# Kernel optimization log

Hardware: AMD Instinct MI355X
Metric: run time of the kernel (lower is better)

## Reference

```python
import jax, jax.numpy as jnp
import numpy as np
import math

B, S, D = 1, 2048, 2048
H, HD, KV = 16, 128, 1
E, F, TOPK = 8, 4096, 2
EPS = 1e-5


def setup_inputs() -> dict:
    key = jax.random.key(0)
    ks = jax.random.split(key, 14)
    sc = 0.02
    inp = {
        "x": jax.random.normal(ks[0], (B, S, D), dtype=jnp.float32),
        "wq": jax.random.normal(ks[1], (D, H * HD), dtype=jnp.float32) * sc,
        "wk": jax.random.normal(ks[2], (D, KV * HD), dtype=jnp.float32) * sc,
        "wv": jax.random.normal(ks[3], (D, KV * HD), dtype=jnp.float32) * sc,
        "wo": jax.random.normal(ks[4], (H * HD, D), dtype=jnp.float32) * sc,
        "w_router": jax.random.normal(ks[5], (D, E), dtype=jnp.float32) * sc,
        "w1": jax.random.normal(ks[6], (E, D, F), dtype=jnp.float32) * sc,
        "w3": jax.random.normal(ks[7], (E, D, F), dtype=jnp.float32) * sc,
        "w2": jax.random.normal(ks[8], (E, F, D), dtype=jnp.float32) * sc,
        "s_pre_mqa": jnp.ones((D,), dtype=jnp.float32),
        "s_post_mqa": jnp.ones((D,), dtype=jnp.float32),
        "s_pre_moe": jnp.ones((D,), dtype=jnp.float32),
        "s_post_moe": jnp.ones((D,), dtype=jnp.float32),
    }
    return inp


def _rmsnorm(x, scale):
    ms = jnp.mean(x * x, axis=-1, keepdims=True)
    return x * jax.lax.rsqrt(ms + EPS) * scale


def _mqa(h, wq, wk, wv, wo):
    b, s, _ = h.shape
    q = (h @ wq).reshape(b, s, H, HD)
    k = (h @ wk).reshape(b, s, KV, HD)
    v = (h @ wv).reshape(b, s, KV, HD)
    # repeat_interleave kv heads up to H (MQA)
    k = jnp.repeat(k, H // KV, axis=2)
    v = jnp.repeat(v, H // KV, axis=2)
    scale = 1.0 / math.sqrt(HD)
    scores = jnp.einsum("bqhd,bkhd->bhqk", q, k) * scale  # [B,H,S,S]
    causal = jnp.tril(jnp.ones((s, s), dtype=bool))
    scores = jnp.where(causal, scores, jnp.float32(-jnp.inf))
    attn = jax.nn.softmax(scores, axis=-1)
    out = jnp.einsum("bhqk,bkhd->bqhd", attn, v).reshape(b, s, H * HD)
    return out @ wo


def _moe(h, w_router, w1, w2, w3):
    logits = h @ w_router                        # [B,S,E]
    probs = jax.nn.softmax(logits, axis=-1)
    topv, topi = jax.lax.top_k(probs, TOPK)      # [B,S,K]
    topv = topv / jnp.sum(topv, axis=-1, keepdims=True)
    # combine weights per expert: [B,S,E]
    combine = jnp.sum(jax.nn.one_hot(topi, E, dtype=h.dtype) * topv[..., None], axis=-2)
    out = jnp.zeros_like(h)
    for e in range(E):  # fixed small expert count
        ye = (jax.nn.silu(h @ w1[e]) * (h @ w3[e])) @ w2[e]
        out = out + combine[..., e:e + 1] * ye
    return out, combine


def reference(x, wq, wk, wv, wo, w_router, w1, w2, w3,
              s_pre_mqa, s_post_mqa, s_pre_moe, s_post_moe):
    mqa_out = _mqa(_rmsnorm(x, s_pre_mqa), wq, wk, wv, wo)
    x = x + _rmsnorm(mqa_out, s_post_mqa)  # dropout p=0 (eval)
    moe_out, router_mask = _moe(_rmsnorm(x, s_pre_moe), w_router, w1, w2, w3)
    x = x + _rmsnorm(moe_out, s_post_moe)
    return x, router_mask
```

## Files before the change

kernel.cpp:

```cpp
#include <hip/hip_runtime.h>

#define S_LEN 2048
#define DM 2048
#define NHEAD 16
#define HDIM 128
#define NEXP 8
#define FF 4096
#define EPSV 1e-5f

typedef unsigned short u16;
typedef short bf16x8 __attribute__((ext_vector_type(8)));
typedef float f32x4 __attribute__((ext_vector_type(4)));

__device__ __forceinline__ f32x4 mfma16(bf16x8 a, bf16x8 b, f32x4 c) {
  return __builtin_amdgcn_mfma_f32_16x16x32_bf16(a, b, c, 0, 0, 0);
}

__device__ __forceinline__ float bf2f(u16 u) {
  union { unsigned int i; float f; } v; v.i = ((unsigned int)u) << 16; return v.f;
}
__device__ __forceinline__ u16 f2bf(float f) {
  union { float f; unsigned int i; } v; v.f = f;
  unsigned int u = v.i;
  return (u16)((u + 0x7fffu + ((u >> 16) & 1u)) >> 16);
}

__device__ __forceinline__ void gload_lds16(const u16* g, u16* l) {
  __builtin_amdgcn_global_load_lds(
      (const __attribute__((address_space(1))) unsigned int*)(unsigned long long)g,
      (__attribute__((address_space(3))) unsigned int*)(unsigned long long)l, 16, 0, 0);
}

__device__ __forceinline__ float blocksum(float v, float* sh) {
#pragma unroll
  for (int off = 32; off; off >>= 1) v += __shfl_xor(v, off, 64);
  const int w = threadIdx.x >> 6;
  if ((threadIdx.x & 63) == 0) sh[w] = v;
  __syncthreads();
  v = sh[0] + sh[1] + sh[2] + sh[3];
  __syncthreads();
  return v;
}

__device__ __forceinline__ void convsplit_body(char* lds, const float* __restrict__ src,
                                               int ld, u16* __restrict__ dhi,
                                               u16* __restrict__ dlo, int nblk, int kblk) {
  float(*tile)[65] = reinterpret_cast<float(*)[65]>(lds);
  const int n0 = nblk * 64, k0 = kblk * 64;
  const int t = threadIdx.x;
  {
    int r = t >> 4, c4 = (t & 15) * 4;
#pragma unroll
    for (int i = 0; i < 4; ++i) {
      float4 v = *reinterpret_cast<const float4*>(src + (size_t)(k0 + r + i * 16) * ld + n0 + c4);
      tile[r + i * 16][c4 + 0] = v.x;
      tile[r + i * 16][c4 + 1] = v.y;
      tile[r + i * 16][c4 + 2] = v.z;
      tile[r + i * 16][c4 + 3] = v.w;
    }
  }
  __syncthreads();
#pragma unroll
  for (int i = 0; i < 2; ++i) {
    int idx = i * 256 + t;
    int n = idx >> 3, kc = (idx & 7) * 8;
    bf16x8 hi, lo;
#pragma unroll
    for (int j = 0; j < 8; ++j) {
      float f = tile[kc + j][n];
      u16 hv = f2bf(f);
      hi[j] = (short)hv;
      lo[j] = (short)f2bf(f - bf2f(hv));
    }
    size_t o = (size_t)(n0 + n) * 2048 + k0 + kc;
    *reinterpret_cast<bf16x8*>(dhi + o) = hi;
    *reinterpret_cast<bf16x8*>(dlo + o) = lo;
  }
}

__device__ __forceinline__ void convT_body(char* lds, const float* __restrict__ src,
                                           int R, int C, u16* __restrict__ dst,
                                           int nblk, int rblk, int e) {
  float(*tile)[65] = reinterpret_cast<float(*)[65]>(lds);
  const int n0 = nblk * 64, r0 = rblk * 64;
  const size_t bofs = (size_t)e * R * C;
  const int t = threadIdx.x;
  {
    int r = t >> 4, c4 = (t & 15) * 4;
#pragma unroll
    for (int i = 0; i < 4; ++i) {
      float4 v = *reinterpret_cast<const float4*>(src + bofs + (size_t)(r0 + r + i * 16) * C + n0 + c4);
      tile[r + i * 16][c4 + 0] = v.x;
      tile[r + i * 16][c4 + 1] = v.y;
      tile[r + i * 16][c4 + 2] = v.z;
      tile[r + i * 16][c4 + 3] = v.w;
    }
  }
  __syncthreads();
#pragma unroll
  for (int i = 0; i < 2; ++i) {
    int idx = i * 256 + t;
    int n = idx >> 3, kc = (idx & 7) * 8;
    bf16x8 pk;
#pragma unroll
    for (int j = 0; j < 8; ++j) pk[j] = (short)f2bf(tile[kc + j][n]);
    *reinterpret_cast<bf16x8*>(dst + bofs + (size_t)(n0 + n) * R + r0 + kc) = pk;
  }
}

__device__ __forceinline__ void convT_body512(char* lds, const float* __restrict__ src,
                                              int R, int C, u16* __restrict__ dst,
                                              int nblk, int rblk, int e) {
  float(*tile)[65] = reinterpret_cast<float(*)[65]>(lds);
  const int n0 = nblk * 64, r0 = rblk * 64;
  const size_t bofs = (size_t)e * R * C;
  const int t = threadIdx.x;
#pragma unroll
  for (int i = 0; i < 2; ++i) {
    int p = i * 512 + t;
    int r = p >> 4, c4 = (p & 15) * 4;
    float4 v = *reinterpret_cast<const float4*>(src + bofs + (size_t)(r0 + r) * C + n0 + c4);
    tile[r][c4 + 0] = v.x;
    tile[r][c4 + 1] = v.y;
    tile[r][c4 + 2] = v.z;
    tile[r][c4 + 3] = v.w;
  }
  __syncthreads();
  {
    int n = t >> 3, kc = (t & 7) * 8;
    bf16x8 pk;
#pragma unroll
    for (int j = 0; j < 8; ++j) pk[j] = (short)f2bf(tile[kc + j][n]);
    *reinterpret_cast<bf16x8*>(dst + bofs + (size_t)(n0 + n) * R + r0 + kc) = pk;
  }
}

__device__ __forceinline__ void rms_pre_body(char* lds, const float* __restrict__ x,
                                             const float* __restrict__ s,
                                             u16* __restrict__ h1, int row) {
  float* sh = (float*)lds;
  const int t = threadIdx.x;
  const float* xr = x + (size_t)row * DM + t * 8;
  float4 a = *reinterpret_cast<const float4*>(xr);
  float4 b = *reinterpret_cast<const float4*>(xr + 4);
  float v[8] = {a.x, a.y, a.z, a.w, b.x, b.y, b.z, b.w};
  float ss = 0.f;
#pragma unroll
  for (int j = 0; j < 8; ++j) ss += v[j] * v[j];
  float inv = rsqrtf(blocksum(ss, sh) * (1.f / DM) + EPSV);
  const float* sp = s + t * 8;
  bf16x8 hi, lo;
#pragma unroll
  for (int j = 0; j < 8; ++j) {
    float val = v[j] * inv * sp[j];
    u16 hv = f2bf(val);
    hi[j] = (short)hv;
    lo[j] = (short)f2bf(val - bf2f(hv));
  }
  *reinterpret_cast<bf16x8*>(h1 + (size_t)row * 4096 + t * 8) = hi;
  *reinterpret_cast<bf16x8*>(h1 + (size_t)row * 4096 + 2048 + t * 8) = lo;
}

__global__ __launch_bounds__(256) void fat_pre(
    const float* __restrict__ x, const float* __restrict__ spre, u16* __restrict__ h1,
    const float* __restrict__ wq, const float* __restrict__ wk, const float* __restrict__ wv,
    u16* __restrict__ BtqHi, u16* __restrict__ BtqLo) {
  __shared__ alignas(16) char lds[16640];
  int bid = blockIdx.x;
  if (bid < 2048) {
    rms_pre_body(lds, x, spre, h1, bid);
  } else if (bid < 3072) {
    int c = bid - 2048;
    convsplit_body(lds, wq, 2048, BtqHi, BtqLo, c & 31, c >> 5);
  } else if (bid < 3136) {
    int c = bid - 3072;
    convsplit_body(lds, wk, 128, BtqHi + (size_t)2048 * 2048, BtqLo + (size_t)2048 * 2048,
                   c & 1, c >> 1);
  } else {
    int c = bid - 3136;
    convsplit_body(lds, wv, 128, BtqHi + (size_t)2176 * 2048, BtqLo + (size_t)2176 * 2048,
                   c & 1, c >> 1);
  }
}

__device__ __forceinline__ void gemm3_body(
    char* lds, const u16* __restrict__ A, const u16* __restrict__ Bthi,
    const u16* __restrict__ Btlo, void* __restrict__ out,
    int mblk, int nblk, int mode, int ldc, int lo_off) {
  const int m0 = mblk * 128, n0 = nblk * 64;
  const int t = threadIdx.x, lane = t & 63, w = t >> 6;
  const int wm = (w >> 1) * 64, wn = (w & 1) * 32;
  const int l15 = lane & 15, lg = lane >> 4;
  const int wbase = t & ~63;

  u16* Ah = (u16*)lds;
  u16* Al = (u16*)(lds + 16384);
  u16* Bh = (u16*)(lds + 32768);
  u16* Bl = (u16*)(lds + 40960);

  const u16* Abh = A + (size_t)m0 * 4096;
  const u16* Abl = Abh + 2048;
  const u16* Bbh = Bthi + (size_t)n0 * 2048;
  const u16* Bbl = Btlo + (size_t)n0 * 2048;

  f32x4 acc[4][2];
#pragma unroll
  for (int m = 0; m < 4; ++m)
#pragma unroll
    for (int n = 0; n < 2; ++n) acc[m][n] = (f32x4){0.f, 0.f, 0.f, 0.f};

  for (int k0 = 0; k0 < 2048; k0 += 64) {
    __syncthreads();
#pragma unroll
    for (int i = 0; i < 4; ++i) {
      int p = i * 256 + t;
      int row = p >> 3;
      int csrc = (p & 7) ^ (row & 7);
      gload_lds16(Abh + (size_t)row * 4096 + k0 + csrc * 8, Ah + (i * 256 + wbase) * 8);
      gload_lds16(Abl + (size_t)row * 4096 + k0 + csrc * 8, Al + (i * 256 + wbase) * 8);
    }
#pragma unroll
    for (int i = 0; i < 2; ++i) {
      int p = i * 256 + t;
      int row = p >> 3;
      int csrc = (p & 7) ^ (row & 7);
      gload_lds16(Bbh + (size_t)row * 2048 + k0 + csrc * 8, Bh + (i * 256 + wbase) * 8);
      gload_lds16(Bbl + (size_t)row * 2048 + k0 + csrc * 8, Bl + (i * 256 + wbase) * 8);
    }
    __syncthreads();
#pragma unroll
    for (int kk = 0; kk < 2; ++kk) {
      bf16x8 ah[4], al[4], bh[2], bl[2];
#pragma unroll
      for (int m = 0; m < 4; ++m) {
        int row = wm + m * 16 + l15;
        int byte = row * 128 + (((kk * 4 + lg) * 16) ^ ((row & 7) << 4));
        ah[m] = *reinterpret_cast<const bf16x8*>((const char*)Ah + byte);
        al[m] = *reinterpret_cast<const bf16x8*>((const char*)Al + byte);
      }
#pragma unroll
      for (int n = 0; n < 2; ++n) {
        int row = wn + n * 16 + l15;
        int byte = row * 128 + (((kk * 4 + lg) * 16) ^ ((row & 7) << 4));
        bh[n] = *reinterpret_cast<const bf16x8*>((const char*)Bh + byte);
        bl[n] = *reinterpret_cast<const bf16x8*>((const char*)Bl + byte);
      }
#pragma unroll
      for (int m = 0; m < 4; ++m)
#pragma unroll
        for (int n = 0; n < 2; ++n) {
          acc[m][n] = mfma16(ah[m], bh[n], acc[m][n]);
          acc[m][n] = mfma16(al[m], bh[n], acc[m][n]);
          acc[m][n] = mfma16(ah[m], bl[n], acc[m][n]);
        }
    }
  }
#pragma unroll
  for (int m = 0; m < 4; ++m)
#pragma unroll
    for (int n = 0; n < 2; ++n)
#pragma unroll
      for (int r = 0; r < 4; ++r) {
        int row = m0 + wm + m * 16 + lg * 4 + r;
        int col = n0 + wn + n * 16 + l15;
        float v = acc[m][n][r];
        if (mode == 1) {
          u16* C = (u16*)out;
          u16 hv = f2bf(v);
          C[(size_t)row * ldc + col] = hv;
          C[(size_t)row * ldc + lo_off + col] = f2bf(v - bf2f(hv));
        } else {
          ((float*)out)[(size_t)row * ldc + col] = v;
        }
      }
}

__global__ __launch_bounds__(256) void fat_qkv_conv(
    const u16* __restrict__ A, const u16* __restrict__ Bthi, const u16* __restrict__ Btlo,
    u16* __restrict__ QKV, const float* __restrict__ w1, u16* __restrict__ w1t,
    const float* __restrict__ wo, u16* __restrict__ BtoHi, u16* __restrict__ BtoLo) {
  __shared__ alignas(16) char lds[49152];
  int bid = blockIdx.x;
  if (bid < 576) {
    gemm3_body(lds, A, Bthi, Btlo, QKV, bid % 16, bid / 16, 1, 4608, 2304);
  } else {
    int cid = bid - 576;
    if (cid < 16384)
      convT_body(lds, w1, 2048, 4096, w1t, cid % 64, (cid / 64) % 32, cid / 2048);
    else {
      cid -= 16384;
      convsplit_body(lds, wo, 2048, BtoHi, BtoLo, cid & 31, cid >> 5);
    }
  }
}

__global__ __launch_bounds__(256) void vtrans_kernel(const u16* __restrict__ QKV,
                                                     u16* __restrict__ vt) {
  __shared__ u16 tile[64][65];
  const int s0 = blockIdx.x * 64, c0 = blockIdx.y * 64;
  const int t = threadIdx.x;
#pragma unroll
  for (int i = 0; i < 16; ++i) {
    int idx = i * 256 + t;
    int r = idx >> 6, c = idx & 63;
    int col = c0 + c;
    int src = (col < 128) ? (2176 + col) : (4480 + col - 128);
    tile[r][c] = QKV[(size_t)(s0 + r) * 4608 + src];
  }
  __syncthreads();
#pragma unroll
  for (int i = 0; i < 16; ++i) {
    int idx = i * 256 + t;
    int cc = idx >> 6, ss = idx & 63;
    vt[(size_t)(c0 + cc) * S_LEN + s0 + ss] = tile[ss][cc];
  }
}

__device__ __forceinline__ void attn_body(char* lds, const u16* __restrict__ QKV,
                                          const u16* __restrict__ vt, u16* __restrict__ Os,
                                          int bx, int h) {
  const int qb = 31 - bx;
  const int t = threadIdx.x, w = t >> 6, lane = t & 63;
  const int l15 = lane & 15, lg = lane >> 4;
  const int qr0 = qb * 64 + w * 16;
  const int qrow = qr0 + l15;

  u16* Ks = (u16*)lds;
  u16* Vs = (u16*)(lds + 17408);
  u16* myP = (u16*)(lds + 37888) + w * (16 * 72);

  bf16x8 qf[2][4];
#pragma unroll
  for (int p = 0; p < 2; ++p)
#pragma unroll
    for (int c = 0; c < 4; ++c)
      qf[p][c] = *reinterpret_cast<const bf16x8*>(QKV + (size_t)qrow * 4608 + p * 2304 +
                                                  h * 128 + c * 32 + lg * 8);

  f32x4 o[8];
#pragma unroll
  for (int n = 0; n < 8; ++n) o[n] = (f32x4){0.f, 0.f, 0.f, 0.f};
  f32x4 lracc = (f32x4){0.f, 0.f, 0.f, 0.f};
  bf16x8 onesf;
#pragma unroll
  for (int j = 0; j < 8; ++j) onesf[j] = (short)0x3F80;

  const float scale = 0.08838834764831845f;
  const int kend = qb * 64 + 64;

  for (int j0 = 0; j0 < kend; j0 += 32) {
    __syncthreads();
#pragma unroll
    for (int i = 0; i < 4; ++i) {
      int idx = i * 256 + t;
      int row = idx >> 5, seg = idx & 31;
      int srccol = (seg < 16) ? (2048 + seg * 8) : (4352 + (seg - 16) * 8);
      bf16x8 v = *reinterpret_cast<const bf16x8*>(QKV + (size_t)(j0 + row) * 4608 + srccol);
      *reinterpret_cast<bf16x8*>(&Ks[row * 272 + seg * 8]) = v;
    }
#pragma unroll
    for (int i = 0; i < 4; ++i) {
      int idx = i * 256 + t;
      int row = idx >> 2, seg = idx & 3;
      bf16x8 v = *reinterpret_cast<const bf16x8*>(vt + (size_t)row * S_LEN + j0 + seg * 8);
      *reinterpret_cast<bf16x8*>(&Vs[row * 40 + seg * 8]) = v;
    }
    __syncthreads();

    if (j0 > qr0 + 15) continue;
    f32x4 sc[2];
#pragma unroll
    for (int half = 0; half < 2; ++half) {
      const int kb = (half * 16 + l15) * 272;
      f32x4 a0 = (f32x4){0.f, 0.f, 0.f, 0.f};
      f32x4 a1 = (f32x4){0.f, 0.f, 0.f, 0.f};
      f32x4 a2 = (f32x4){0.f, 0.f, 0.f, 0.f};
#pragma unroll
      for (int cc = 0; cc < 4; ++cc) {
        bf16x8 kh = *reinterpret_cast<const bf16x8*>(&Ks[kb + cc * 32 + lg * 8]);
        a0 = mfma16(qf[0][cc], kh, a0);
        a1 = mfma16(qf[1][cc], kh, a1);
      }
#pragma unroll
      for (int cc = 0; cc < 4; ++cc) {
        bf16x8 kl = *reinterpret_cast<const bf16x8*>(&Ks[kb + 128 + cc * 32 + lg * 8]);
        a2 = mfma16(qf[0][cc], kl, a2);
      }
      f32x4 a = (a0 + a1) + a2;
#pragma unroll
      for (int r = 0; r < 4; ++r) {
        int rowg = qr0 + lg * 4 + r;
        int colg = j0 + half * 16 + l15;
        sc[half][r] = (colg <= rowg) ? a[r] * scale : -1e30f;
      }
    }
#pragma unroll
    for (int r = 0; r < 4; ++r) {
      float p0 = __expf(sc[0][r]);
      float p1 = __expf(sc[1][r]);
      int lrow = lg * 4 + r;
      u16 h0 = f2bf(p0), h1v = f2bf(p1);
      myP[lrow * 72 + l15] = h0;
      myP[lrow * 72 + 16 + l15] = h1v;
      myP[lrow * 72 + 32 + l15] = f2bf(p0 - bf2f(h0));
      myP[lrow * 72 + 48 + l15] = f2bf(p1 - bf2f(h1v));
    }
    bf16x8 pfh = *reinterpret_cast<const bf16x8*>(myP + l15 * 72 + lg * 8);
    bf16x8 pfl = *reinterpret_cast<const bf16x8*>(myP + l15 * 72 + 32 + lg * 8);

    lracc = mfma16(pfh, onesf, lracc);
    lracc = mfma16(pfl, onesf, lracc);

#pragma unroll
    for (int n = 0; n < 8; ++n) {
      bf16x8 vh = *reinterpret_cast<const bf16x8*>(&Vs[(n * 16 + l15) * 40 + lg * 8]);
      bf16x8 vl = *reinterpret_cast<const bf16x8*>(&Vs[(n * 16 + l15 + 128) * 40 + lg * 8]);
      o[n] = mfma16(pfh, vh, o[n]);
      o[n] = mfma16(pfl, vh, o[n]);
      o[n] = mfma16(pfh, vl, o[n]);
    }
  }
#pragma unroll
  for (int n = 0; n < 8; ++n)
#pragma unroll
    for (int r = 0; r < 4; ++r) {
      int rowg = qr0 + lg * 4 + r;
      float v = o[n][r] / lracc[r];
      u16 hv = f2bf(v);
      Os[(size_t)rowg * 4096 + h * 128 + n * 16 + l15] = hv;
      Os[(size_t)rowg * 4096 + 2048 + h * 128 + n * 16 + l15] = f2bf(v - bf2f(hv));
    }
}

__global__ __launch_bounds__(256) void fat_attn_conv(
    const u16* __restrict__ QKV, const u16* __restrict__ vt, u16* __restrict__ Os,
    const float* __restrict__ w3, u16* __restrict__ w3t) {
  __shared__ alignas(16) char lds[47104];
  int bid = blockIdx.x;
  if (bid < 512) {
    attn_body(lds, QKV, vt, Os, bid & 31, bid >> 5);
  } else {
    int cid = bid - 512;
    convT_body(lds, w3, 2048, 4096, w3t, cid % 64, (cid / 64) % 32, cid / 2048);
  }
}

__global__ __launch_bounds__(256) void fat_wo_conv(
    const u16* __restrict__ A, const u16* __restrict__ Bthi, const u16* __restrict__ Btlo,
    float* __restrict__ out, const float* __restrict__ w2, u16* __restrict__ w2t) {
  __shared__ alignas(16) char lds[49152];
  int bid = blockIdx.x;
  if (bid < 512) {
    gemm3_body(lds, A, Bthi, Btlo, out, bid & 15, bid >> 4, 2, 2048, 0);
  } else {
    int cid = bid - 512;
    convT_body(lds, w2, 4096, 2048, w2t, cid % 32, (cid / 32) % 64, cid / 2048);
  }
}

__global__ __launch_bounds__(256) void rms_mid_router(
    const float* __restrict__ x, const float* __restrict__ mqa,
    const float* __restrict__ spost, const float* __restrict__ spre,
    const float* __restrict__ wr, float* __restrict__ x1, u16* __restrict__ h2b,
    float* __restrict__ comb, int* __restrict__ topi, float* __restrict__ topw,
    int* __restrict__ cnt) {
  __shared__ float sh1[4];
  __shared__ float sh2[4];
  __shared__ float red[4][8];
  __shared__ float lgits[8];
  const int row = blockIdx.x, t = threadIdx.x;
  const size_t base = (size_t)row * DM + t * 8;
  float mv[8];
  {
    float4 a0 = *reinterpret_cast<const float4*>(mqa + base);
    float4 b0 = *reinterpret_cast<const float4*>(mqa + base + 4);
    mv[0] = a0.x; mv[1] = a0.y; mv[2] = a0.z; mv[3] = a0.w;
    mv[4] = b0.x; mv[5] = b0.y; mv[6] = b0.z; mv[7] = b0.w;
  }
  float ss1 = 0.f;
#pragma unroll
  for (int j = 0; j < 8; ++j) ss1 += mv[j] * mv[j];
  float inv1 = rsqrtf(blocksum(ss1, sh1) * (1.f / DM) + EPSV);
  float4 xa = *reinterpret_cast<const float4*>(x + base);
  float4 xb = *reinterpret_cast<const float4*>(x + base + 4);
  float xv[8] = {xa.x, xa.y, xa.z, xa.w, xb.x, xb.y, xb.z, xb.w};
  float x1v[8];
  float ss2 = 0.f;
#pragma unroll
  for (int j = 0; j < 8; ++j) {
    x1v[j] = xv[j] + mv[j] * inv1 * spost[t * 8 + j];
    ss2 += x1v[j] * x1v[j];
  }
  float inv2 = rsqrtf(blocksum(ss2, sh2) * (1.f / DM) + EPSV);
  *reinterpret_cast<float4*>(x1 + base) = make_float4(x1v[0], x1v[1], x1v[2], x1v[3]);
  *reinterpret_cast<float4*>(x1 + base + 4) = make_float4(x1v[4], x1v[5], x1v[6], x1v[7]);
  float hv[8];
  bf16x8 hb;
#pragma unroll
  for (int j = 0; j < 8; ++j) {
    hv[j] = x1v[j] * inv2 * spre[t * 8 + j];
    hb[j] = (short)f2bf(hv[j]);
  }
  *reinterpret_cast<bf16x8*>(h2b + base) = hb;

  float acc[8] = {0.f, 0.f, 0.f, 0.f, 0.f, 0.f, 0.f, 0.f};
  const float* wrow = wr + (size_t)t * 64;
#pragma unroll
  for (int j = 0; j < 8; ++j) {
    const float* wj = wrow + j * 8;
#pragma unroll
    for (int e = 0; e < 8; ++e) acc[e] += hv[j] * wj[e];
  }
#pragma unroll
  for (int off = 32; off; off >>= 1)
#pragma unroll
    for (int e = 0; e < 8; ++e) acc[e] += __shfl_xor(acc[e], off, 64);
  const int w = t >> 6;
  if ((t & 63) == 0) {
#pragma unroll
    for (int e = 0; e < 8; ++e) red[w][e] = acc[e];
  }
  __syncthreads();
  if (t < 8) lgits[t] = red[0][t] + red[1][t] + red[2][t] + red[3][t];
  __syncthreads();
  if (t == 0) {
    float L[8], mx = -1e30f;
#pragma unroll
    for (int e = 0; e < 8; ++e) {
      L[e] = lgits[e];
      mx = fmaxf(mx, L[e]);
    }
    float p[8], s = 0.f;
#pragma unroll
    for (int e = 0; e < 8; ++e) {
      p[e] = expf(L[e] - mx);
      s += p[e];
    }
#pragma unroll
    for (int e = 0; e < 8; ++e) p[e] /= s;
    int e0 = 0;
    for (int e = 1; e < 8; ++e)
      if (p[e] > p[e0]) e0 = e;
    int e1 = (e0 == 0) ? 1 : 0;
    for (int e = 0; e < 8; ++e)
      if (e != e0 && p[e] > p[e1]) e1 = e;
    float ssum = p[e0] + p[e1];
    float w0 = p[e0] / ssum, w1 = p[e1] / ssum;
    for (int e = 0; e < 8; ++e)
      comb[(size_t)row * 8 + e] = (e == e0) ? w0 : ((e == e1) ? w1 : 0.f);
    topi[2 * row] = e0;
    topi[2 * row + 1] = e1;
    topw[2 * row] = w0;
    topw[2 * row + 1] = w1;
    atomicAdd(&cnt[e0], 1);
    atomicAdd(&cnt[e1], 1);
  }
}

__global__ void zero_meta_kernel(int* __restrict__ cnt) {
  if (threadIdx.x < NEXP) cnt[threadIdx.x] = 0;
}

__global__ void build_meta_kernel(const int* __restrict__ cnt, int* __restrict__ cursor,
                                  int* __restrict__ meta, int* __restrict__ meta128) {
  if (threadIdx.x != 0) return;
  int off = 0, nt = 0, nt2 = 0;
  for (int e = 0; e < NEXP; ++e) {
    int c = cnt[e];
    cursor[e] = off;
    int ntl = (c + 255) >> 8;
    for (int r = 0; r < ntl; ++r) {
      meta[8 + nt] = e;
      meta[64 + nt] = off + r * 256;
      int rem = c - r * 256;
      meta[120 + nt] = rem < 256 ? rem : 256;
      ++nt;
    }
    int ntl2 = (c + 127) >> 7;
    for (int r = 0; r < ntl2; ++r) {
      meta128[8 + nt2] = e;
      meta128[64 + nt2] = off + r * 128;
      int rem = c - r * 128;
      meta128[120 + nt2] = rem < 128 ? rem : 128;
      ++nt2;
    }
    off += c;
  }
  meta[0] = nt;
  meta128[0] = nt2;
}

__global__ void scatter_kernel(const int* __restrict__ topi, int* __restrict__ cursor,
                               int* __restrict__ ptok, int* __restrict__ pos_of) {
  int token = blockIdx.x * 256 + threadIdx.x;
  if (token >= S_LEN) return;
  for (int k = 0; k < 2; ++k) {
    int e = topi[2 * token + k];
    int pos = atomicAdd(&cursor[e], 1);
    ptok[pos] = token;
    pos_of[2 * token + k] = pos;
  }
}

__device__ __forceinline__ void moe_gemm1_body(
    char* lds, const u16* __restrict__ H2, const u16* __restrict__ W1t,
    const u16* __restrict__ W3t, u16* __restrict__ U, const int* __restrict__ meta,
    const int* __restrict__ ptok, int tile, int n0blk) {
  if (tile >= meta[0]) return;
  u16* As = (u16*)lds;
  u16* B1s = (u16*)(lds + 16384);
  u16* B3s = (u16*)(lds + 24576);
  int* toks = (int*)(lds + 32768);
  const int e = meta[8 + tile], row0 = meta[64 + tile], rows = meta[120 + tile];
  const int n0 = n0blk * 64;
  const u16* B1 = W1t + (size_t)e * FF * DM + (size_t)n0 * 2048;
  const u16* B3 = W3t + (size_t)e * FF * DM + (size_t)n0 * 2048;
  const int t = threadIdx.x, lane = t & 63, w = t >> 6;
  const int wm = (w >> 2) * 64, wn = (w & 3) * 16;
  const int l15 = lane & 15, lg = lane >> 4;
  const int wbase = t & ~63;

  if (t < 128) toks[t] = (t < rows) ? ptok[row0 + t] : ptok[row0];
  __syncthreads();

  f32x4 aG[4], aT[4];
#pragma unroll
  for (int m = 0; m < 4; ++m) {
    aG[m] = (f32x4){0.f, 0.f, 0.f, 0.f};
    aT[m] = (f32x4){0.f, 0.f, 0.f, 0.f};
  }

  for (int k0 = 0; k0 < DM; k0 += 64) {
    __syncthreads();
#pragma unroll
    for (int i = 0; i < 2; ++i) {
      int p = i * 512 + t;
      int row = p >> 3;
      int csrc = (p & 7) ^ (row & 7);
      gload_lds16(H2 + (size_t)toks[row] * DM + k0 + csrc * 8, As + (i * 512 + wbase) * 8);
    }
    {
      int row = t >> 3;
      int csrc = (t & 7) ^ (row & 7);
      gload_lds16(B1 + (size_t)row * 2048 + k0 + csrc * 8, B1s + wbase * 8);
      gload_lds16(B3 + (size_t)row * 2048 + k0 + csrc * 8, B3s + wbase * 8);
    }
    __syncthreads();
#pragma unroll
    for (int kk = 0; kk < 2; ++kk) {
      bf16x8 af[4], b1f, b3f;
#pragma unroll
      for (int m = 0; m < 4; ++m) {
        int row = wm + m * 16 + l15;
        int byte = row * 128 + (((kk * 4 + lg) * 16) ^ ((row & 7) << 4));
        af[m] = *reinterpret_cast<const bf16x8*>((const char*)As + byte);
      }
      {
        int row = wn + l15;
        int byte = row * 128 + (((kk * 4 + lg) * 16) ^ ((row & 7) << 4));
        b1f = *reinterpret_cast<const bf16x8*>((const char*)B1s + byte);
        b3f = *reinterpret_cast<const bf16x8*>((const char*)B3s + byte);
      }
#pragma unroll
      for (int m = 0; m < 4; ++m) {
        aG[m] = mfma16(af[m], b1f, aG[m]);
        aT[m] = mfma16(af[m], b3f, aT[m]);
      }
    }
  }
#pragma unroll
  for (int m = 0; m < 4; ++m)
#pragma unroll
    for (int r = 0; r < 4; ++r) {
      int lrow = wm + m * 16 + lg * 4 + r;
      if (lrow < rows) {
        float g = aG[m][r], tt = aT[m][r];
        float u = (g / (1.f + __expf(-g))) * tt;
        U[(size_t)(row0 + lrow) * FF + n0 + wn + l15] = f2bf(u);
      }
    }
}

__global__ __launch_bounds__(512) void fat_moe1(
    const u16* __restrict__ H2, const u16* __restrict__ W1t, const u16* __restrict__ W3t,
    u16* __restrict__ U, const int* __restrict__ meta128, const int* __restrict__ ptok,
    const float* __restrict__ w2, u16* __restrict__ w2t) {
  __shared__ alignas(16) char lds[33280];
  int bid = blockIdx.x;
  if (bid < 2560) {
    moe_gemm1_body(lds, H2, W1t, W3t, U, meta128, ptok, bid >> 6, bid & 63);
  } else {
    int cid = bid - 2560;
    convT_body512(lds, w2, 4096, 2048, w2t, cid % 32, (cid / 32) % 64, 4 + cid / 2048);
  }
}

__global__ __launch_bounds__(512) void moe_gemm2b(
    const u16* __restrict__ U, const u16* __restrict__ W2t, u16* __restrict__ Y,
    const int* __restrict__ meta128) {
  const int tile = blockIdx.x;
  if (tile >= meta128[0]) return;
  const int e = meta128[8 + tile], row0 = meta128[64 + tile], rows = meta128[120 + tile];
  const int n0 = blockIdx.y * 128;
  const u16* Bb = W2t + (size_t)e * DM * FF + (size_t)n0 * 4096;
  const int t = threadIdx.x, lane = t & 63, w = t >> 6;
  const int wm = (w >> 2) * 64, wn = (w & 3) * 32;
  const int l15 = lane & 15, lg = lane >> 4;
  const int wbase = t & ~63;

  __shared__ alignas(16) u16 As[8192];
  __shared__ alignas(16) u16 Bs[8192];

  f32x4 acc[4][2];
#pragma unroll
  for (int m = 0; m < 4; ++m)
#pragma unroll
    for (int n = 0; n < 2; ++n) acc[m][n] = (f32x4){0.f, 0.f, 0.f, 0.f};

  for (int k0 = 0; k0 < FF; k0 += 64) {
    __syncthreads();
#pragma unroll
    for (int i = 0; i < 2; ++i) {
      int p = i * 512 + t;
      int row = p >> 3;
      int csrc = (p & 7) ^ (row & 7);
      gload_lds16(U + (size_t)(row0 + row) * FF + k0 + csrc * 8, As + (i * 512 + wbase) * 8);
    }
#pragma unroll
    for (int i = 0; i < 2; ++i) {
      int p = i * 512 + t;
      int row = p >> 3;
      int csrc = (p & 7) ^ (row & 7);
      gload_lds16(Bb + (size_t)row * 4096 + k0 + csrc * 8, Bs + (i * 512 + wbase) * 8);
    }
    __syncthreads();
#pragma unroll
    for (int kk = 0; kk < 2; ++kk) {
      bf16x8 af[4], bfr[2];
#pragma unroll
      for (int m = 0; m < 4; ++m) {
        int row = wm + m * 16 + l15;
        int byte = row * 128 + (((kk * 4 + lg) * 16) ^ ((row & 7) << 4));
        af[m] = *reinterpret_cast<const bf16x8*>((const char*)As + byte);
      }
#pragma unroll
      for (int n = 0; n < 2; ++n) {
        int row = wn + n * 16 + l15;
        int byte = row * 128 + (((kk * 4 + lg) * 16) ^ ((row & 7) << 4));
        bfr[n] = *reinterpret_cast<const bf16x8*>((const char*)Bs + byte);
      }
#pragma unroll
      for (int m = 0; m < 4; ++m)
#pragma unroll
        for (int n = 0; n < 2; ++n) acc[m][n] = mfma16(af[m], bfr[n], acc[m][n]);
    }
  }
#pragma unroll
  for (int m = 0; m < 4; ++m)
#pragma unroll
    for (int n = 0; n < 2; ++n)
#pragma unroll
      for (int r = 0; r < 4; ++r) {
        int lrow = wm + m * 16 + lg * 4 + r;
        if (lrow < rows)
          Y[(size_t)(row0 + lrow) * DM + n0 + wn + n * 16 + l15] = f2bf(acc[m][n][r]);
      }
}

__global__ __launch_bounds__(256) void moe_final_kernel(
    const float* __restrict__ x1, const u16* __restrict__ Y,
    const int* __restrict__ pos_of, const float* __restrict__ topw,
    const float* __restrict__ spost, float* __restrict__ xout) {
  __shared__ float sh[4];
  const int row = blockIdx.x, t = threadIdx.x;
  const int p0 = pos_of[2 * row], p1 = pos_of[2 * row + 1];
  const float w0 = topw[2 * row], w1 = topw[2 * row + 1];
  bf16x8 y0 = *reinterpret_cast<const bf16x8*>(Y + (size_t)p0 * DM + t * 8);
  bf16x8 y1 = *reinterpret_cast<const bf16x8*>(Y + (size_t)p1 * DM + t * 8);
  float mv[8];
  float ss = 0.f;
#pragma unroll
  for (int j = 0; j < 8; ++j) {
    mv[j] = w0 * bf2f((u16)y0[j]) + w1 * bf2f((u16)y1[j]);
    ss += mv[j] * mv[j];
  }
  float inv = rsqrtf(blocksum(ss, sh) * (1.f / DM) + EPSV);
  const size_t base = (size_t)row * DM + t * 8;
#pragma unroll
  for (int j = 0; j < 8; ++j)
    xout[base + j] = x1[base + j] + mv[j] * inv * spost[t * 8 + j];
}

extern "C" void kernel_launch(void* const* d_in, const int* in_sizes, int n_in,
                              void* d_out, int out_size, void* d_ws, size_t ws_size,
                              hipStream_t stream) {
  (void)in_sizes; (void)n_in; (void)out_size; (void)ws_size;
  const float* x = (const float*)d_in[0];
  const float* wq = (const float*)d_in[1];
  const float* wk = (const float*)d_in[2];
  const float* wv = (const float*)d_in[3];
  const float* wo = (const float*)d_in[4];
  const float* wrt = (const float*)d_in[5];
  const float* w1 = (const float*)d_in[6];
  const float* w3 = (const float*)d_in[7];
  const float* w2 = (const float*)d_in[8];
  const float* s_pre_mqa = (const float*)d_in[9];
  const float* s_post_mqa = (const float*)d_in[10];
  const float* s_pre_moe = (const float*)d_in[11];
  const float* s_post_moe = (const float*)d_in[12];

  float* xout = (float*)d_out;
  float* out_router = xout + (size_t)S_LEN * DM;

  char* wsp = (char*)d_ws;
  size_t off = 0;
  auto alloc = [&](size_t n) {
    char* p = wsp + off;
    off += (n + 255) & ~(size_t)255;
    return p;
  };
  u16* U = (u16*)alloc((size_t)4096 * FF * 2);
  u16* Y = (u16*)alloc((size_t)4096 * DM * 2);
  float* mqa = (float*)alloc((size_t)S_LEN * DM * 4);
  u16* h1s = (u16*)alloc((size_t)S_LEN * 4096 * 2);
  u16* attn_s = h1s;
  u16* Btq_hi = (u16*)alloc((size_t)2304 * 2048 * 2);
  u16* Btq_lo = (u16*)alloc((size_t)2304 * 2048 * 2);
  u16* Bto_hi = (u16*)alloc((size_t)2048 * 2048 * 2);
  u16* Bto_lo = (u16*)alloc((size_t)2048 * 2048 * 2);
  u16* QKV = (u16*)alloc((size_t)S_LEN * 4608 * 2);
  u16* vt = (u16*)alloc((size_t)256 * S_LEN * 2);
  float* x1 = (float*)alloc((size_t)S_LEN * DM * 4);
  u16* h2b = (u16*)alloc((size_t)S_LEN * DM * 2);
  int* topi = (int*)alloc(4096 * 4);
  float* topw = (float*)alloc(4096 * 4);
  int* pos_of = (int*)alloc(4096 * 4);
  int* ptok = (int*)alloc(4352 * 4);
  int* cnt = (int*)alloc(32 * 4);
  int* cursor = (int*)alloc(32 * 4);
  int* meta = (int*)alloc(256 * 4);
  int* meta128 = (int*)alloc(256 * 4);
  u16* w1t = (u16*)alloc((size_t)NEXP * DM * FF * 2);
  u16* w3t = (u16*)alloc((size_t)NEXP * DM * FF * 2);
  u16* w2t = (u16*)alloc((size_t)NEXP * FF * DM * 2);

  dim3 B256(256);
  dim3 B512(512);

  fat_pre<<<dim3(3200), B256, 0, stream>>>(x, s_pre_mqa, h1s, wq, wk, wv, Btq_hi, Btq_lo);
  fat_qkv_conv<<<dim3(576 + 16384 + 1024), B256, 0, stream>>>(
      h1s, Btq_hi, Btq_lo, QKV, w1, w1t, wo, Bto_hi, Bto_lo);
  vtrans_kernel<<<dim3(32, 4), B256, 0, stream>>>(QKV, vt);
  fat_attn_conv<<<dim3(512 + 16384), B256, 0, stream>>>(QKV, vt, attn_s, w3, w3t);
  fat_wo_conv<<<dim3(512 + 8192), B256, 0, stream>>>(attn_s, Bto_hi, Bto_lo, mqa, w2, w2t);
  zero_meta_kernel<<<dim3(1), dim3(64), 0, stream>>>(cnt);
  rms_mid_router<<<dim3(S_LEN), B256, 0, stream>>>(x, mqa, s_post_mqa, s_pre_moe, wrt,
                                                   x1, h2b, out_router, topi, topw, cnt);
  build_meta_kernel<<<dim3(1), dim3(64), 0, stream>>>(cnt, cursor, meta, meta128);
  scatter_kernel<<<dim3(8), B256, 0, stream>>>(topi, cursor, ptok, pos_of);
  fat_moe1<<<dim3(2560 + 8192), B512, 0, stream>>>(h2b, w1t, w3t, U, meta128, ptok, w2, w2t);
  moe_gemm2b<<<dim3(40, 16), B512, 0, stream>>>(U, w2t, Y, meta128);
  moe_final_kernel<<<dim3(S_LEN), B256, 0, stream>>>(x1, Y, pos_of, topw, s_post_moe, xout);
}
```

Baseline: 780.1 us.

## Move second half of w2 conversion from MoE gemm1 kernel into wo kernel

The w2 weight transpose/convert blocks for experts 4-7 are no longer fused into the MoE gemm1 launch. Instead the wo projection kernel's grid is doubled so it converts all of w2, and gemm1 becomes a standalone kernel with a 2D grid. The aim is to overlap conversion work with the small wo GEMM, which underfills the GPU, rather than with the heavier gemm1. The cost is a longer wo stage, and it assumes fat_wo_conv's block indexing covers all eight experts.

```diff
diff --git a/kernel.cpp b/kernel.cpp
--- a/kernel.cpp
+++ b/kernel.cpp
@@ -101,33 +101,6 @@
   for (int i = 0; i < 2; ++i) {
     int idx = i * 256 + t;
     int n = idx >> 3, kc = (idx & 7) * 8;
-    bf16x8 pk;
-#pragma unroll
-    for (int j = 0; j < 8; ++j) pk[j] = (short)f2bf(tile[kc + j][n]);
-    *reinterpret_cast<bf16x8*>(dst + bofs + (size_t)(n0 + n) * R + r0 + kc) = pk;
-  }
-}
-
-__device__ __forceinline__ void convT_body512(char* lds, const float* __restrict__ src,
-                                              int R, int C, u16* __restrict__ dst,
-                                              int nblk, int rblk, int e) {
-  float(*tile)[65] = reinterpret_cast<float(*)[65]>(lds);
-  const int n0 = nblk * 64, r0 = rblk * 64;
-  const size_t bofs = (size_t)e * R * C;
-  const int t = threadIdx.x;
-#pragma unroll
-  for (int i = 0; i < 2; ++i) {
-    int p = i * 512 + t;
-    int r = p >> 4, c4 = (p & 15) * 4;
-    float4 v = *reinterpret_cast<const float4*>(src + bofs + (size_t)(r0 + r) * C + n0 + c4);
-    tile[r][c4 + 0] = v.x;
-    tile[r][c4 + 1] = v.y;
-    tile[r][c4 + 2] = v.z;
-    tile[r][c4 + 3] = v.w;
-  }
-  __syncthreads();
-  {
-    int n = t >> 3, kc = (t & 7) * 8;
     bf16x8 pk;
 #pragma unroll
     for (int j = 0; j < 8; ++j) pk[j] = (short)f2bf(tile[kc + j][n]);
@@ -602,17 +575,18 @@
   }
 }
 
-__device__ __forceinline__ void moe_gemm1_body(
-    char* lds, const u16* __restrict__ H2, const u16* __restrict__ W1t,
-    const u16* __restrict__ W3t, u16* __restrict__ U, const int* __restrict__ meta,
-    const int* __restrict__ ptok, int tile, int n0blk) {
+__global__ __launch_bounds__(512) void moe_gemm1k(
+    const u16* __restrict__ H2, const u16* __restrict__ W1t, const u16* __restrict__ W3t,
+    u16* __restrict__ U, const int* __restrict__ meta, const int* __restrict__ ptok) {
+  const int tile = blockIdx.x;
   if (tile >= meta[0]) return;
+  __shared__ alignas(16) char lds[33280];
   u16* As = (u16*)lds;
   u16* B1s = (u16*)(lds + 16384);
   u16* B3s = (u16*)(lds + 24576);
   int* toks = (int*)(lds + 32768);
   const int e = meta[8 + tile], row0 = meta[64 + tile], rows = meta[120 + tile];
-  const int n0 = n0blk * 64;
+  const int n0 = blockIdx.y * 64;
   const u16* B1 = W1t + (size_t)e * FF * DM + (size_t)n0 * 2048;
   const u16* B3 = W3t + (size_t)e * FF * DM + (size_t)n0 * 2048;
   const int t = threadIdx.x, lane = t & 63, w = t >> 6;
@@ -679,20 +653,6 @@
         U[(size_t)(row0 + lrow) * FF + n0 + wn + l15] = f2bf(u);
       }
     }
-}
-
-__global__ __launch_bounds__(512) void fat_moe1(
-    const u16* __restrict__ H2, const u16* __restrict__ W1t, const u16* __restrict__ W3t,
-    u16* __restrict__ U, const int* __restrict__ meta128, const int* __restrict__ ptok,
-    const float* __restrict__ w2, u16* __restrict__ w2t) {
-  __shared__ alignas(16) char lds[33280];
-  int bid = blockIdx.x;
-  if (bid < 2560) {
-    moe_gemm1_body(lds, H2, W1t, W3t, U, meta128, ptok, bid >> 6, bid & 63);
-  } else {
-    int cid = bid - 2560;
-    convT_body512(lds, w2, 4096, 2048, w2t, cid % 32, (cid / 32) % 64, 4 + cid / 2048);
-  }
 }
 
 __global__ __launch_bounds__(512) void moe_gemm2b(
@@ -852,13 +812,13 @@
       h1s, Btq_hi, Btq_lo, QKV, w1, w1t, wo, Bto_hi, Bto_lo);
   vtrans_kernel<<<dim3(32, 4), B256, 0, stream>>>(QKV, vt);
   fat_attn_conv<<<dim3(512 + 16384), B256, 0, stream>>>(QKV, vt, attn_s, w3, w3t);
-  fat_wo_conv<<<dim3(512 + 8192), B256, 0, stream>>>(attn_s, Bto_hi, Bto_lo, mqa, w2, w2t);
+  fat_wo_conv<<<dim3(512 + 16384), B256, 0, stream>>>(attn_s, Bto_hi, Bto_lo, mqa, w2, w2t);
   zero_meta_kernel<<<dim3(1), dim3(64), 0, stream>>>(cnt);
   rms_mid_router<<<dim3(S_LEN), B256, 0, stream>>>(x, mqa, s_post_mqa, s_pre_moe, wrt,
                                                    x1, h2b, out_router, topi, topw, cnt);
   build_meta_kernel<<<dim3(1), dim3(64), 0, stream>>>(cnt, cursor, meta, meta128);
   scatter_kernel<<<dim3(8), B256, 0, stream>>>(topi, cursor, ptok, pos_of);
-  fat_moe1<<<dim3(2560 + 8192), B512, 0, stream>>>(h2b, w1t, w3t, U, meta128, ptok, w2, w2t);
+  moe_gemm1k<<<dim3(40, 64), B512, 0, stream>>>(h2b, w1t, w3t, U, meta128, ptok);
   moe_gemm2b<<<dim3(40, 16), B512, 0, stream>>>(U, w2t, Y, meta128);
   moe_final_kernel<<<dim3(S_LEN), B256, 0, stream>>>(x1, Y, pos_of, topw, s_post_moe, xout);
 }
```

Measured after the change: 847.5 us. 1.09x slower.
